# Kernel optimization log

Hardware: AMD Instinct MI355X
Metric: run time of the kernel (lower is better)

The kernel has to match this reference:

```python
import jax, jax.numpy as jnp
import numpy as np

NEG = -1e30  # finite stand-in for -inf (avoids NaN grads in logsumexp of all-impossible states)


def _ctc_loss(logp, targets, lengths, blank=0):
    """CTC loss, mean reduction (per-sample loss / target_length, then batch mean).
    logp: [B, T, V] log-probabilities; targets: [B, S] labels (no blanks); lengths: [B].
    All input lengths are T (matches preds_size = [T]*batch_size in the original).
    """
    B, T, V = logp.shape
    S = targets.shape[1]
    Sx = 2 * S + 1
    # extended label sequence: blank, l1, blank, l2, ..., blank
    ext = jnp.zeros((B, Sx), dtype=targets.dtype).at[:, 1::2].set(targets)
    prev2 = jnp.pad(ext, ((0, 0), (2, 0)))[:, :Sx]
    skip = (ext != blank) & (ext != prev2)  # [B, Sx] allow s-2 transition
    # gather emission log-probs for extended labels: [B, T, Sx] -> [T, B, Sx]
    emit = jnp.take_along_axis(logp, ext[:, None, :], axis=2)
    emit = jnp.transpose(emit, (1, 0, 2))
    alpha0 = jnp.full((B, Sx), NEG, logp.dtype)
    alpha0 = alpha0.at[:, 0].set(emit[0, :, 0]).at[:, 1].set(emit[0, :, 1])
    neg1 = jnp.full((B, 1), NEG, logp.dtype)
    neg2 = jnp.full((B, 2), NEG, logp.dtype)

    def step(alpha, emit_t):
        a1 = alpha
        a2 = jnp.concatenate([neg1, alpha[:, :-1]], axis=1)
        a3 = jnp.where(skip, jnp.concatenate([neg2, alpha[:, :-2]], axis=1), NEG)
        m = jnp.maximum(a1, jnp.maximum(a2, a3))
        lse = m + jnp.log(jnp.exp(a1 - m) + jnp.exp(a2 - m) + jnp.exp(a3 - m))
        return lse + emit_t, None

    alpha, _ = jax.lax.scan(step, alpha0, emit[1:])  # [B, Sx] at t = T-1
    i2 = (2 * lengths).astype(jnp.int32)
    a_end = jnp.take_along_axis(alpha, jnp.stack([i2 - 1, i2], axis=1), axis=1)  # [B, 2]
    ll = jax.nn.logsumexp(a_end, axis=1)
    loss = -ll
    loss = jnp.where(jnp.isfinite(loss), loss, jnp.zeros_like(loss))  # zero_infinity
    return jnp.mean(loss / lengths.astype(logp.dtype))  # reduction='mean'


def setup_inputs() -> dict:
    key = jax.random.key(0)
    k1, k2, k3 = jax.random.split(key, 3)
    B, T, V, S = 64, 256, 6625, 25
    pred = jax.random.normal(k1, (B, T, V), dtype=jnp.float32)
    target = jax.random.randint(k2, (B, S), 1, V)  # labels exclude blank=0
    length = jax.random.randint(k3, (B,), 1, S + 1)
    return {"pred": pred, "target": target, "length": length, "batch_size": B}


def reference(pred, target, length, batch_size):
    logp = jax.nn.log_softmax(pred, axis=2)
    return _ctc_loss(logp, target, length, blank=0)
```

## Files before the change

### kernel.cpp

```cpp
#include <hip/hip_runtime.h>
#include <math.h>

#define NEGV (-1e30f)

constexpr int Bc = 64;
constexpr int Tc = 256;
constexpr int Vc = 6625;
constexpr int Sc = 25;
constexpr int SX = 2 * Sc + 1;
constexpr int NV4 = Vc / 4;
constexpr int EMITK = Sc + 1;
constexpr int EMIT_ROW = Tc * EMITK;

__global__ __launch_bounds__(256) void k_lse_gather(const float* __restrict__ pred,
                                                    const int* __restrict__ target,
                                                    float* __restrict__ emit) {
    const int bid = blockIdx.x;
    const int b = bid >> 8;
    const int tid = threadIdx.x;
    const float* __restrict__ row = pred + (size_t)bid * Vc;
    const float4* __restrict__ row4 = (const float4*)row;

    float4 v[7];
#pragma unroll
    for (int j = 0; j < 7; ++j) {
        int f = tid + j * 256;
        if (f < NV4) v[j] = row4[f];
        else v[j] = make_float4(-INFINITY, -INFINITY, -INFINITY, -INFINITY);
    }
    float tailv = (tid == 0) ? row[Vc - 1] : -INFINITY;

    float m = tailv;
#pragma unroll
    for (int j = 0; j < 7; ++j)
        m = fmaxf(m, fmaxf(fmaxf(v[j].x, v[j].y), fmaxf(v[j].z, v[j].w)));
#pragma unroll
    for (int off = 1; off < 64; off <<= 1)
        m = fmaxf(m, __shfl_xor(m, off));

    __shared__ float smax[4];
    __shared__ float ssum[4];
    const int wave = tid >> 6, lane = tid & 63;
    if (lane == 0) smax[wave] = m;
    __syncthreads();
    const float M = fmaxf(fmaxf(smax[0], smax[1]), fmaxf(smax[2], smax[3]));

    float s = (tid == 0) ? expf(tailv - M) : 0.0f;
#pragma unroll
    for (int j = 0; j < 7; ++j)
        s += expf(v[j].x - M) + expf(v[j].y - M) + expf(v[j].z - M) + expf(v[j].w - M);
#pragma unroll
    for (int off = 1; off < 64; off <<= 1)
        s += __shfl_xor(s, off);
    if (lane == 0) ssum[wave] = s;
    __syncthreads();
    const float lse = M + logf(ssum[0] + ssum[1] + ssum[2] + ssum[3]);

    if (tid < EMITK) {
        int col = (tid == 0) ? 0 : target[b * Sc + (tid - 1)];
        emit[(size_t)bid * EMITK + tid] = row[col] - lse;
    }
}

__global__ __launch_bounds__(256) void k_ctc(const float* __restrict__ emit,
                                             const int* __restrict__ target,
                                             const int* __restrict__ length,
                                             float* __restrict__ lossb) {
    __shared__ float lds[EMIT_ROW];
    const int b = blockIdx.x;
    const int tid = threadIdx.x;

    const float4* __restrict__ src4 = (const float4*)(emit + (size_t)b * EMIT_ROW);
    float4* dst4 = (float4*)lds;
#pragma unroll
    for (int j = 0; j < 7; ++j) {
        int f = tid + j * 256;
        if (f < EMIT_ROW / 4) dst4[f] = src4[f];
    }
    __syncthreads();
    if (tid >= 64) return;

    const int lane = tid;
    int k = (lane & 1) ? ((lane >> 1) + 1) : 0;
    if (lane >= SX) k = 0;

    bool skip = false;
    if ((lane & 1) && lane >= 3 && lane < SX) {
        int cur = target[b * Sc + ((lane - 1) >> 1)];
        int prev = target[b * Sc + ((lane - 3) >> 1)];
        skip = (cur != 0) && (cur != prev);
    }

    float alpha = (lane <= 1) ? lds[k] : NEGV;
    if (lane >= SX) alpha = NEGV;

    float et = lds[EMITK + k];
#pragma unroll 4
    for (int t = 1; t < Tc; ++t) {
        float et_n = (t + 1 < Tc) ? lds[(t + 1) * EMITK + k] : 0.0f;
        float a1 = alpha;
        float a2 = __shfl_up(alpha, 1);
        float a3 = __shfl_up(alpha, 2);
        if (lane < 1) a2 = NEGV;
        if (lane < 2 || !skip) a3 = NEGV;
        float m = fmaxf(a1, fmaxf(a2, a3));
        float l = m + logf(expf(a1 - m) + expf(a2 - m) + expf(a3 - m));
        alpha = l + et;
        if (lane >= SX) alpha = NEGV;
        et = et_n;
    }

    const int len = length[b];
    const int i2 = 2 * len;
    float ae0 = __shfl(alpha, i2 - 1);
    float ae1 = __shfl(alpha, i2);
    float mm = fmaxf(ae0, ae1);
    float ll = mm + logf(expf(ae0 - mm) + expf(ae1 - mm));
    float loss = -ll;
    if (!isfinite(loss)) loss = 0.0f;
    if (lane == 0) lossb[b] = loss / (float)len;
}

__global__ __launch_bounds__(64) void k_final(const float* __restrict__ lossb,
                                              float* __restrict__ out) {
    float v = lossb[threadIdx.x];
#pragma unroll
    for (int off = 1; off < 64; off <<= 1)
        v += __shfl_xor(v, off);
    if (threadIdx.x == 0) out[0] = v * (1.0f / 64.0f);
}

extern "C" void kernel_launch(void* const* d_in, const int* in_sizes, int n_in,
                              void* d_out, int out_size, void* d_ws, size_t ws_size,
                              hipStream_t stream) {
    const float* pred   = (const float*)d_in[0];
    const int*   target = (const int*)d_in[1];
    const int*   length = (const int*)d_in[2];

    float* emit  = (float*)d_ws;
    float* lossb = emit + (size_t)Bc * EMIT_ROW;

    k_lse_gather<<<Bc * Tc, 256, 0, stream>>>(pred, target, emit);
    k_ctc<<<Bc, 256, 0, stream>>>(emit, target, length, lossb);
    k_final<<<1, 64, 0, stream>>>(lossb, (float*)d_out);
}
```

Before: 615.5 us.

## Drop max pass in softmax LSE, work in base-2 with hardware exp2/log2

```diff
diff --git a/kernel.cpp b/kernel.cpp
--- a/kernel.cpp
+++ b/kernel.cpp
@@ -8,57 +8,57 @@
 constexpr int Vc = 6625;
 constexpr int Sc = 25;
 constexpr int SX = 2 * Sc + 1;
-constexpr int NV4 = Vc / 4;
 constexpr int EMITK = Sc + 1;
 constexpr int EMIT_ROW = Tc * EMITK;
+
+constexpr float LOG2E = 1.4426950408889634f;
+constexpr float LN2   = 0.6931471805599453f;
 
 __global__ __launch_bounds__(256) void k_lse_gather(const float* __restrict__ pred,
                                                     const int* __restrict__ target,
                                                     float* __restrict__ emit) {
-    const int bid = blockIdx.x;
-    const int b = bid >> 8;
+    const int R = blockIdx.x;
+    const int b = R >> 8;
     const int tid = threadIdx.x;
-    const float* __restrict__ row = pred + (size_t)bid * Vc;
-    const float4* __restrict__ row4 = (const float4*)row;
+    const float* __restrict__ row = pred + (size_t)R * Vc;
 
-    float4 v[7];
+    const int lead = (4 - (R & 3)) & 3;
+    const int n4   = (Vc - lead) >> 2;
+    const int tail = (Vc - lead) & 3;
+    const float4* __restrict__ row4 = (const float4*)(row + lead);
+
+    float s = 0.0f;
+    if (tid < lead) s += __builtin_amdgcn_exp2f(row[tid] * LOG2E);
+    if (tid < tail) s += __builtin_amdgcn_exp2f(row[lead + 4 * n4 + tid] * LOG2E);
+
 #pragma unroll
     for (int j = 0; j < 7; ++j) {
         int f = tid + j * 256;
-        if (f < NV4) v[j] = row4[f];
-        else v[j] = make_float4(-INFINITY, -INFINITY, -INFINITY, -INFINITY);
+        if (f < n4) {
+            float4 v = row4[f];
+            s += __builtin_amdgcn_exp2f(v.x * LOG2E)
+               + __builtin_amdgcn_exp2f(v.y * LOG2E)
+               + __builtin_amdgcn_exp2f(v.z * LOG2E)
+               + __builtin_amdgcn_exp2f(v.w * LOG2E);
+        }
     }
-    float tailv = (tid == 0) ? row[Vc - 1] : -INFINITY;
 
-    float m = tailv;
-#pragma unroll
-    for (int j = 0; j < 7; ++j)
-        m = fmaxf(m, fmaxf(fmaxf(v[j].x, v[j].y), fmaxf(v[j].z, v[j].w)));
-#pragma unroll
-    for (int off = 1; off < 64; off <<= 1)
-        m = fmaxf(m, __shfl_xor(m, off));
-
-    __shared__ float smax[4];
-    __shared__ float ssum[4];
-    const int wave = tid >> 6, lane = tid & 63;
-    if (lane == 0) smax[wave] = m;
-    __syncthreads();
-    const float M = fmaxf(fmaxf(smax[0], smax[1]), fmaxf(smax[2], smax[3]));
-
-    float s = (tid == 0) ? expf(tailv - M) : 0.0f;
-#pragma unroll
-    for (int j = 0; j < 7; ++j)
-        s += expf(v[j].x - M) + expf(v[j].y - M) + expf(v[j].z - M) + expf(v[j].w - M);
 #pragma unroll
     for (int off = 1; off < 64; off <<= 1)
         s += __shfl_xor(s, off);
+
+    __shared__ float ssum[4];
+    __shared__ float slse;
+    const int wave = tid >> 6, lane = tid & 63;
     if (lane == 0) ssum[wave] = s;
     __syncthreads();
-    const float lse = M + logf(ssum[0] + ssum[1] + ssum[2] + ssum[3]);
+    if (tid == 0) slse = __builtin_amdgcn_logf(ssum[0] + ssum[1] + ssum[2] + ssum[3]);
+    __syncthreads();
+    const float lse2 = slse;
 
     if (tid < EMITK) {
         int col = (tid == 0) ? 0 : target[b * Sc + (tid - 1)];
-        emit[(size_t)bid * EMITK + tid] = row[col] - lse;
+        emit[(size_t)R * EMITK + tid] = row[col] * LOG2E - lse2;
     }
 }
 
@@ -86,7 +86,7 @@
 
     bool skip = false;
     if ((lane & 1) && lane >= 3 && lane < SX) {
-        int cur = target[b * Sc + ((lane - 1) >> 1)];
+        int cur  = target[b * Sc + ((lane - 1) >> 1)];
         int prev = target[b * Sc + ((lane - 3) >> 1)];
         skip = (cur != 0) && (cur != prev);
     }
@@ -103,9 +103,11 @@
         float a3 = __shfl_up(alpha, 2);
         if (lane < 1) a2 = NEGV;
         if (lane < 2 || !skip) a3 = NEGV;
-        float m = fmaxf(a1, fmaxf(a2, a3));
-        float l = m + logf(expf(a1 - m) + expf(a2 - m) + expf(a3 - m));
-        alpha = l + et;
+        float m = fmaxf(fmaxf(a1, a2), a3);
+        float sum = __builtin_amdgcn_exp2f(a1 - m)
+                  + __builtin_amdgcn_exp2f(a2 - m)
+                  + __builtin_amdgcn_exp2f(a3 - m);
+        alpha = m + __builtin_amdgcn_logf(sum) + et;
         if (lane >= SX) alpha = NEGV;
         et = et_n;
     }
@@ -115,8 +117,9 @@
     float ae0 = __shfl(alpha, i2 - 1);
     float ae1 = __shfl(alpha, i2);
     float mm = fmaxf(ae0, ae1);
-    float ll = mm + logf(expf(ae0 - mm) + expf(ae1 - mm));
-    float loss = -ll;
+    float ll2 = mm + __builtin_amdgcn_logf(__builtin_amdgcn_exp2f(ae0 - mm)
+                                         + __builtin_amdgcn_exp2f(ae1 - mm));
+    float loss = -ll2 * LN2;
     if (!isfinite(loss)) loss = 0.0f;
     if (lane == 0) lossb[b] = loss / (float)len;
 }
```

New measurement: 582.5 us. 5.4% less time.
